# Kernel optimization log

Hardware: AMD Instinct MI355X
Metric: run time of the kernel (lower is better)

## Reference

```python
import jax, jax.numpy as jnp
import numpy as np

B, C, H, W = 8, 64, 256, 256


def setup_inputs() -> dict:
    key = jax.random.key(0)
    ks = jax.random.split(key, 7)
    return {
        "x": jax.random.normal(ks[0], (B, C, H, W), dtype=jnp.float32),
        "query_w": jax.random.normal(ks[1], (C, W, W), dtype=jnp.float32),
        "key_w": jax.random.normal(ks[2], (C, W, W), dtype=jnp.float32),
        "var_w": jax.random.normal(ks[3], (C, W, W), dtype=jnp.float32),
        "query_b": jax.random.normal(ks[4], (C, H, W), dtype=jnp.float32),
        "key_b": jax.random.normal(ks[5], (C, H, W), dtype=jnp.float32),
        "var_b": jax.random.normal(ks[6], (C, H, W), dtype=jnp.float32),
    }


def reference(x, query_w, key_w, var_w, query_b, key_b, var_b):
    # mode == 'horizontal': per-channel right-matmul over the W axis.
    # x: [B,C,H,W], *_w: [C,W,W] (broadcast over batch), *_b: [C,H,W].
    q = jnp.einsum("bchw,cwv->bchv", x, query_w) + query_b
    k = jnp.einsum("bchw,cwv->bchv", x, key_w) + key_b
    v = jnp.einsum("bchw,cwv->bchv", x, var_w) + var_b
    return jax.nn.softmax(q * k, axis=-1) * v
```

## Files before the change

kernel.cpp:

```cpp
#include <hip/hip_runtime.h>
#include <math.h>


#define Bn 8
#define Cn 64
#define Hn 256
#define Wn 256

typedef _Float16 f16x8 __attribute__((ext_vector_type(8)));
typedef _Float16 f16x4 __attribute__((ext_vector_type(4)));
typedef float    f32x16 __attribute__((ext_vector_type(16)));

#define MFMA(a, b, c) __builtin_amdgcn_mfma_f32_32x32x16_f16((a), (b), (c), 0, 0, 0)

#define WS_PLANE_H 4096
#define WS_NEED ((size_t)Cn * 16 * 5 * 8192)

#define FPL  8192
#define FBUF 40960

__device__ __forceinline__ void ldst16(const void* g, void* l) {
    __builtin_amdgcn_global_load_lds(
        (const __attribute__((address_space(1))) unsigned int*)g,
        (__attribute__((address_space(3))) unsigned int*)l, 16, 0, 0);
}

__device__ __forceinline__ void cvt_hilo(const float4 a, const float4 b,
                                         f16x8& hi, f16x8& lo) {
    float v[8] = {a.x, a.y, a.z, a.w, b.x, b.y, b.z, b.w};
#pragma unroll
    for (int e = 0; e < 8; ++e) {
        _Float16 hv = (_Float16)v[e];
        hi[e] = hv;
        lo[e] = (_Float16)(v[e] - (float)hv);
    }
}

__global__ __launch_bounds__(256) void prep_w(
    const float* __restrict__ wq, const float* __restrict__ wk,
    const float* __restrict__ wv, _Float16* __restrict__ wf)
{
    const int blk = blockIdx.x;
    const int kt  = blk & 15;
    const int c   = blk >> 4;
    const int n   = threadIdx.x;
    const int ntile = n >> 5;
    const int nl    = n & 31;

    _Float16* base = wf + (size_t)blk * 5 * WS_PLANE_H;
    const size_t woff = ((size_t)c * Wn + kt * 16) * Wn + n;

#pragma unroll
    for (int mat = 0; mat < 2; ++mat) {
        const float* Wp = (mat ? wk : wq) + woff;
        float w16[16];
#pragma unroll
        for (int r = 0; r < 16; ++r)
            w16[r] = Wp[(size_t)r * Wn];
        _Float16* hip = base + (mat * 2) * WS_PLANE_H + ntile * 512;
        _Float16* lop = hip + WS_PLANE_H;
#pragma unroll
        for (int h2 = 0; h2 < 2; ++h2) {
            f16x8 hi8, lo8;
#pragma unroll
            for (int e = 0; e < 8; ++e) {
                const float wv_ = w16[h2 * 8 + e];
                _Float16 hv = (_Float16)wv_;
                hi8[e] = hv;
                lo8[e] = (_Float16)(wv_ - (float)hv);
            }
            *(f16x8*)(hip + (h2 * 32 + nl) * 8) = hi8;
            *(f16x8*)(lop + (h2 * 32 + nl) * 8) = lo8;
        }
    }
    {
        const float* Wp = wv + woff;
        float w16[16];
#pragma unroll
        for (int r = 0; r < 16; ++r)
            w16[r] = Wp[(size_t)r * Wn];
        _Float16* vp = base + 4 * WS_PLANE_H + ntile * 512;
#pragma unroll
        for (int h2 = 0; h2 < 2; ++h2) {
            f16x8 hi8;
#pragma unroll
            for (int e = 0; e < 8; ++e)
                hi8[e] = (_Float16)w16[h2 * 8 + e];
            *(f16x8*)(vp + (h2 * 32 + nl) * 8) = hi8;
        }
    }
}

__global__ __launch_bounds__(512, 4) void axile_attn_fused(
    const float* __restrict__ x,
    const _Float16* __restrict__ wf,
    const float* __restrict__ bq,
    const float* __restrict__ bk,
    const float* __restrict__ bv,
    float* __restrict__ out)
{
    __shared__ __align__(16) char lds[2 * FBUF];

    const int tid  = threadIdx.x;
    const int ncol = tid >> 6;
    const int lane = tid & 63;
    const int h    = lane >> 5;
    const int l31  = lane & 31;

    const int blk = blockIdx.x;
    const int c   = blk & 63;
    const int j   = blk >> 6;
    const int b   = j & 7;
    const int h0  = (j >> 3) * 32;

    const float* xrow = x + ((size_t)(b * Cn + c) * Hn + h0 + l31) * Wn + h * 8;
    const _Float16* wfc = wf + (size_t)c * 16 * 5 * WS_PLANE_H;

    f32x16 accq, acck, accv;
#pragma unroll
    for (int r = 0; r < 16; ++r) {
        accq[r] = 0.f;
        acck[r] = 0.f;
        accv[r] = 0.f;
    }

#pragma unroll
    for (int p = 0; p < 5; ++p)
        ldst16(wfc + p * WS_PLANE_H + tid * 8, lds + p * FPL + tid * 16);
    f16x8 ah, al;
    {
        const float4 xa = *(const float4*)(xrow);
        const float4 xb = *(const float4*)(xrow + 4);
        cvt_hilo(xa, xb, ah, al);
    }
    __syncthreads();

    int curo = 0;
    for (int kt = 0; kt < 16; ++kt) {
        const int nxto = curo ^ FBUF;
        float4 xa, xb;
        if (kt < 15) {
            xa = *(const float4*)(xrow + (kt + 1) * 16);
            xb = *(const float4*)(xrow + (kt + 1) * 16 + 4);
            const _Float16* wsp = wfc + (size_t)(kt + 1) * 5 * WS_PLANE_H;
#pragma unroll
            for (int p = 0; p < 5; ++p)
                ldst16(wsp + p * WS_PLANE_H + tid * 8,
                       lds + nxto + p * FPL + tid * 16);
        }

        const char* bb = lds + curo + ncol * 1024 + lane * 16;
        const f16x8 bqh = *(const f16x8*)(bb + 0 * FPL);
        const f16x8 bql = *(const f16x8*)(bb + 1 * FPL);
        const f16x8 bkh = *(const f16x8*)(bb + 2 * FPL);
        const f16x8 bkl = *(const f16x8*)(bb + 3 * FPL);
        const f16x8 bvh = *(const f16x8*)(bb + 4 * FPL);

        accq = MFMA(ah, bqh, accq);
        accq = MFMA(al, bqh, accq);
        accq = MFMA(ah, bql, accq);
        acck = MFMA(ah, bkh, acck);
        acck = MFMA(al, bkh, acck);
        acck = MFMA(ah, bkl, acck);
        accv = MFMA(ah, bvh, accv);

        if (kt < 15)
            cvt_hilo(xa, xb, ah, al);
        __syncthreads();
        curo = nxto;
    }

    float* part    = (float*)lds;
    float* combmax = (float*)(lds + 1024);
    float* combsum = (float*)(lds + 1152);

#pragma unroll
    for (int r = 0; r < 16; ++r) {
        const int row = (r & 3) + 8 * (r >> 2) + 4 * h;
        const int hh  = h0 + row;
        const int vv  = ncol * 32 + l31;
        const size_t bidx = ((size_t)c * Hn + hh) * Wn + vv;
        const float qv = accq[r] + bq[bidx];
        const float kv = acck[r] + bk[bidx];
        accq[r] = qv * kv;
    }

#pragma unroll
    for (int r = 0; r < 16; ++r) {
        float m2 = accq[r];
#pragma unroll
        for (int off = 16; off > 0; off >>= 1)
            m2 = fmaxf(m2, __shfl_xor(m2, off, 64));
        if ((lane & 31) == r) {
            const int row = (r & 3) + 8 * (r >> 2) + 4 * h;
            part[ncol * 32 + row] = m2;
        }
    }
    __syncthreads();
    if (tid < 32) {
        float m = part[tid];
#pragma unroll
        for (int w = 1; w < 8; ++w)
            m = fmaxf(m, part[w * 32 + tid]);
        combmax[tid] = m;
    }
    __syncthreads();

#pragma unroll
    for (int r = 0; r < 16; ++r) {
        const int row = (r & 3) + 8 * (r >> 2) + 4 * h;
        const float mx = combmax[row];
        const float e0 = __expf(accq[r] - mx);
        accq[r] = e0;
        float ps = e0;
#pragma unroll
        for (int off = 16; off > 0; off >>= 1)
            ps += __shfl_xor(ps, off, 64);
        if ((lane & 31) == r)
            part[ncol * 32 + row] = ps;
    }
    __syncthreads();
    if (tid < 32) {
        float s = part[tid];
#pragma unroll
        for (int w = 1; w < 8; ++w)
            s += part[w * 32 + tid];
        combsum[tid] = s;
    }
    __syncthreads();

    float* obase = out + ((size_t)(b * Cn + c) * Hn) * Wn;
#pragma unroll
    for (int r = 0; r < 16; ++r) {
        const int row = (r & 3) + 8 * (r >> 2) + 4 * h;
        const float inv = 1.0f / combsum[row];
        const int hh = h0 + row;
        const int vv = ncol * 32 + l31;
        const size_t bidx = ((size_t)c * Hn + hh) * Wn + vv;
        const float vx = accv[r] + bv[bidx];
        obase[(size_t)hh * Wn + vv] = accq[r] * vx * inv;
    }
}

#define LDS_ALO 2048
#define LDS_B   4096

__global__ __launch_bounds__(512, 4) void axile_attn_mfma4(
    const float* __restrict__ x,
    const float* __restrict__ wq,
    const float* __restrict__ wk,
    const float* __restrict__ wv,
    const float* __restrict__ bq,
    const float* __restrict__ bk,
    const float* __restrict__ bv,
    float* __restrict__ out)
{
    __shared__ __align__(16) char lds[39424];

    const int tid  = threadIdx.x;
    const int ncol = tid >> 6;
    const int lane = tid & 63;
    const int h    = lane >> 5;
    const int l31  = lane & 31;

    const int blk = blockIdx.x;
    const int c   = blk & 63;
    const int j   = blk >> 6;
    const int b   = j & 7;
    const int h0  = (j >> 3) * 64;

    const float* xbase = x + ((size_t)(b * Cn + c) * Hn + h0) * Wn;
    const float* w_q = wq + (size_t)c * Wn * Wn;
    const float* w_k = wk + (size_t)c * Wn * Wn;
    const float* w_v = wv + (size_t)c * Wn * Wn;

    const int wkh = tid >> 8;
    const int n   = tid & 255;
    const int ntW = n >> 5;
    const int nl  = n & 31;
    const int wfo = ((wkh << 5) | nl) * 16;
    const int am    = tid >> 2;
    const int akq   = tid & 3;
    const int amt   = am >> 5;
    const int alc   = ((akq >> 1) << 5) | (am & 31);
    const int aboff = (akq & 1) * 8;

    f32x16 accq[2], acck[2];
#pragma unroll
    for (int mt = 0; mt < 2; ++mt)
#pragma unroll
        for (int r = 0; r < 16; ++r) {
            accq[mt][r] = 0.f;
            acck[mt][r] = 0.f;
        }

    for (int kt = 0; kt < 16; ++kt) {
        const int k0 = kt * 16;
        __syncthreads();
#pragma unroll
        for (int mat = 0; mat < 2; ++mat) {
            const float* Wp = mat ? w_k : w_q;
            const float* wrow = Wp + (size_t)(k0 + wkh * 8) * Wn + n;
            float w8[8];
#pragma unroll
            for (int r = 0; r < 8; ++r)
                w8[r] = wrow[(size_t)r * Wn];
            f16x8 hi8, lo8;
#pragma unroll
            for (int e = 0; e < 8; ++e) {
                const float wv_ = w8[e];
                _Float16 hv = (_Float16)wv_;
                hi8[e] = hv;
                lo8[e] = (_Float16)(wv_ - (float)hv);
            }
            char* dplane = lds + LDS_B + (mat * 2) * 8192 + ntW * 1024;
            *(f16x8*)(dplane + wfo) = hi8;
            *(f16x8*)(dplane + 8192 + wfo) = lo8;
        }
        if (tid < 256) {
            const float4 xx = *(const float4*)(xbase + (size_t)am * Wn + k0 + akq * 4);
            f16x4 hi4, lo4;
            _Float16 t0 = (_Float16)xx.x; hi4[0] = t0; lo4[0] = (_Float16)(xx.x - (float)t0);
            _Float16 t1 = (_Float16)xx.y; hi4[1] = t1; lo4[1] = (_Float16)(xx.y - (float)t1);
            _Float16 t2 = (_Float16)xx.z; hi4[2] = t2; lo4[2] = (_Float16)(xx.z - (float)t2);
            _Float16 t3 = (_Float16)xx.w; hi4[3] = t3; lo4[3] = (_Float16)(xx.w - (float)t3);
            *(f16x4*)(lds + amt * 1024 + alc * 16 + aboff) = hi4;
            *(f16x4*)(lds + LDS_ALO + amt * 1024 + alc * 16 + aboff) = lo4;
        }
        __syncthreads();

        f16x8 ah[2], al[2];
#pragma unroll
        for (int mt = 0; mt < 2; ++mt) {
            ah[mt] = *(const f16x8*)(lds + mt * 1024 + lane * 16);
            al[mt] = *(const f16x8*)(lds + LDS_ALO + mt * 1024 + lane * 16);
        }
        const char* bb = lds + LDS_B + ncol * 1024 + lane * 16;
        f16x8 bqh = *(const f16x8*)(bb + 0 * 8192);
        f16x8 bql = *(const f16x8*)(bb + 1 * 8192);
        f16x8 bkh = *(const f16x8*)(bb + 2 * 8192);
        f16x8 bkl = *(const f16x8*)(bb + 3 * 8192);
#pragma unroll
        for (int mt = 0; mt < 2; ++mt) {
            accq[mt] = MFMA(ah[mt], bqh, accq[mt]);
            accq[mt] = MFMA(al[mt], bqh, accq[mt]);
            accq[mt] = MFMA(ah[mt], bql, accq[mt]);
            acck[mt] = MFMA(ah[mt], bkh, acck[mt]);
            acck[mt] = MFMA(al[mt], bkh, acck[mt]);
            acck[mt] = MFMA(ah[mt], bkl, acck[mt]);
        }
    }

    float* part    = (float*)(lds + 36864);
    float* combmax = (float*)(lds + 36864 + 2048);
    float* combsum = (float*)(lds + 36864 + 2304);

#pragma unroll
    for (int mt = 0; mt < 2; ++mt)
#pragma unroll
        for (int r = 0; r < 16; ++r) {
            const int rl = (r & 3) + 8 * (r >> 2) + 4 * h;
            const int hh = h0 + mt * 32 + rl;
            const int vv = ncol * 32 + l31;
            const size_t bidx = ((size_t)c * Hn + hh) * Wn + vv;
            const float qv = accq[mt][r] + bq[bidx];
            const float kv = acck[mt][r] + bk[bidx];
            accq[mt][r] = qv * kv;
        }

#pragma unroll
    for (int mt = 0; mt < 2; ++mt)
#pragma unroll
        for (int r = 0; r < 16; ++r) {
            float m2 = accq[mt][r];
#pragma unroll
            for (int off = 16; off > 0; off >>= 1)
                m2 = fmaxf(m2, __shfl_xor(m2, off, 64));
            if ((lane & 15) == r && ((lane >> 4) & 1) == mt) {
                const int rl  = (r & 3) + 8 * (r >> 2) + 4 * h;
                const int row = mt * 32 + rl;
                part[ncol * 64 + row] = m2;
            }
        }
    __syncthreads();
    if (tid < 64) {
        float m = part[tid];
#pragma unroll
        for (int w = 1; w < 8; ++w)
            m = fmaxf(m, part[w * 64 + tid]);
        combmax[tid] = m;
    }
    __syncthreads();

#pragma unroll
    for (int mt = 0; mt < 2; ++mt)
#pragma unroll
        for (int r = 0; r < 16; ++r) {
            const int rl  = (r & 3) + 8 * (r >> 2) + 4 * h;
            const int row = mt * 32 + rl;
            const float mx = combmax[row];
            const float e0 = __expf(accq[mt][r] - mx);
            accq[mt][r] = e0;
            float ps = e0;
#pragma unroll
            for (int off = 16; off > 0; off >>= 1)
                ps += __shfl_xor(ps, off, 64);
            if ((lane & 15) == r && ((lane >> 4) & 1) == mt)
                part[ncol * 64 + row] = ps;
        }
    __syncthreads();
    if (tid < 64) {
        float s = part[tid];
#pragma unroll
        for (int w = 1; w < 8; ++w)
            s += part[w * 64 + tid];
        combsum[tid] = s;
    }

    f32x16 accv[2];
#pragma unroll
    for (int mt = 0; mt < 2; ++mt)
#pragma unroll
        for (int r = 0; r < 16; ++r)
            accv[mt][r] = 0.f;

    for (int kt = 0; kt < 16; ++kt) {
        const int k0 = kt * 16;
        __syncthreads();
        {
            const float* wrow = w_v + (size_t)(k0 + wkh * 8) * Wn + n;
            float w8[8];
#pragma unroll
            for (int r = 0; r < 8; ++r)
                w8[r] = wrow[(size_t)r * Wn];
            f16x8 hi8;
#pragma unroll
            for (int e = 0; e < 8; ++e)
                hi8[e] = (_Float16)w8[e];
            *(f16x8*)(lds + LDS_B + ntW * 1024 + wfo) = hi8;
        }
        if (tid < 256) {
            const float4 xx = *(const float4*)(xbase + (size_t)am * Wn + k0 + akq * 4);
            f16x4 hi4;
            hi4[0] = (_Float16)xx.x;
            hi4[1] = (_Float16)xx.y;
            hi4[2] = (_Float16)xx.z;
            hi4[3] = (_Float16)xx.w;
            *(f16x4*)(lds + amt * 1024 + alc * 16 + aboff) = hi4;
        }
        __syncthreads();

        f16x8 ah[2];
#pragma unroll
        for (int mt = 0; mt < 2; ++mt)
            ah[mt] = *(const f16x8*)(lds + mt * 1024 + lane * 16);
        f16x8 bvh = *(const f16x8*)(lds + LDS_B + ncol * 1024 + lane * 16);
#pragma unroll
        for (int mt = 0; mt < 2; ++mt)
            accv[mt] = MFMA(ah[mt], bvh, accv[mt]);
    }

    float* obase = out + ((size_t)(b * Cn + c) * Hn) * Wn;
#pragma unroll
    for (int mt = 0; mt < 2; ++mt)
#pragma unroll
        for (int r = 0; r < 16; ++r) {
            const int rl  = (r & 3) + 8 * (r >> 2) + 4 * h;
            const int row = mt * 32 + rl;
            const float inv = 1.0f / combsum[row];
            const int hh = h0 + row;
            const int vv = ncol * 32 + l31;
            const size_t bidx = ((size_t)c * Hn + hh) * Wn + vv;
            const float vx = accv[mt][r] + bv[bidx];
            obase[(size_t)hh * Wn + vv] = accq[mt][r] * vx * inv;
        }
}

extern "C" void kernel_launch(void* const* d_in, const int* in_sizes, int n_in,
                              void* d_out, int out_size, void* d_ws, size_t ws_size,
                              hipStream_t stream) {
    (void)in_sizes; (void)n_in; (void)out_size;
    const float* x  = (const float*)d_in[0];
    const float* wq = (const float*)d_in[1];
    const float* wk = (const float*)d_in[2];
    const float* wv = (const float*)d_in[3];
    const float* bq = (const float*)d_in[4];
    const float* bk = (const float*)d_in[5];
    const float* bv = (const float*)d_in[6];
    float* out = (float*)d_out;

    if (d_ws != nullptr && ws_size >= WS_NEED) {
        hipLaunchKernelGGL(prep_w, dim3(Cn * 16), dim3(256), 0, stream,
                           wq, wk, wv, (_Float16*)d_ws);
        hipLaunchKernelGGL(axile_attn_fused, dim3(Bn * 8 * Cn), dim3(512), 0, stream,
                           x, (const _Float16*)d_ws, bq, bk, bv, out);
    } else {
        hipLaunchKernelGGL(axile_attn_mfma4, dim3(Bn * 4 * Cn), dim3(512), 0, stream,
                           x, wq, wk, wv, bq, bk, bv, out);
    }
}
```

Before: 549.0 us.

## Use 1024-thread blocks with 64-row tiles and triple-buffered weight prefetch

The fused kernel now uses 1024 threads covering 64 rows per block, so each staged weight tile is shared by two row groups and global weight traffic per output halves. The double buffer becomes a three-stage ring filled two tiles ahead, with explicit vmcnt waits and raw s_barrier in place of full __syncthreads. The aim is to hide global-to-LDS latency and cut redundant weight loads. The cost is 120KB of LDS per block, which limits residency to one block per CU, plus fragile hand-written waitcnt logic.

```diff
diff --git a/kernel.cpp b/kernel.cpp
--- a/kernel.cpp
+++ b/kernel.cpp
@@ -16,8 +16,7 @@
 #define WS_PLANE_H 4096
 #define WS_NEED ((size_t)Cn * 16 * 5 * 8192)
 
-#define FPL  8192
-#define FBUF 40960
+#define FTILE 40960
 
 __device__ __forceinline__ void ldst16(const void* g, void* l) {
     __builtin_amdgcn_global_load_lds(
@@ -91,7 +90,7 @@
     }
 }
 
-__global__ __launch_bounds__(512, 4) void axile_attn_fused(
+__global__ __launch_bounds__(1024, 4) void axile_attn_pipe(
     const float* __restrict__ x,
     const _Float16* __restrict__ wf,
     const float* __restrict__ bq,
@@ -99,22 +98,29 @@
     const float* __restrict__ bv,
     float* __restrict__ out)
 {
-    __shared__ __align__(16) char lds[2 * FBUF];
-
-    const int tid  = threadIdx.x;
-    const int ncol = tid >> 6;
-    const int lane = tid & 63;
-    const int h    = lane >> 5;
-    const int l31  = lane & 31;
+    __shared__ __align__(16) char lds[3 * FTILE];
+
+    const int tid   = threadIdx.x;
+    const int lane  = tid & 63;
+    const int h     = lane >> 5;
+    const int l31   = lane & 31;
+    const int wv_id = tid >> 6;
+    const int ncol  = wv_id & 7;
+    const int mt    = wv_id >> 3;
 
     const int blk = blockIdx.x;
     const int c   = blk & 63;
     const int j   = blk >> 6;
     const int b   = j & 7;
-    const int h0  = (j >> 3) * 32;
-
-    const float* xrow = x + ((size_t)(b * Cn + c) * Hn + h0 + l31) * Wn + h * 8;
-    const _Float16* wfc = wf + (size_t)c * 16 * 5 * WS_PLANE_H;
+    const int h0  = (j >> 3) * 64;
+
+    const float* xrow = x + ((size_t)(b * Cn + c) * Hn + h0 + mt * 32 + l31) * Wn + h * 8;
+    const char*  wfc  = (const char*)(wf + (size_t)c * 16 * 5 * WS_PLANE_H);
+
+    const bool halfw = (tid < 512);
+    const int  so0 = tid * 16;
+    const int  so1 = 16384 + tid * 16;
+    const int  so2 = 32768 + tid * 16;
 
     f32x16 accq, acck, accv;
 #pragma unroll
@@ -124,37 +130,44 @@
         accv[r] = 0.f;
     }
 
-#pragma unroll
-    for (int p = 0; p < 5; ++p)
-        ldst16(wfc + p * WS_PLANE_H + tid * 8, lds + p * FPL + tid * 16);
     f16x8 ah, al;
     {
         const float4 xa = *(const float4*)(xrow);
         const float4 xb = *(const float4*)(xrow + 4);
+        ldst16(wfc + so0, lds + so0);
+        ldst16(wfc + so1, lds + so1);
+        if (halfw) ldst16(wfc + so2, lds + so2);
+        const char* s1 = wfc + FTILE;
+        ldst16(s1 + so0, lds + FTILE + so0);
+        ldst16(s1 + so1, lds + FTILE + so1);
+        if (halfw) ldst16(s1 + so2, lds + FTILE + so2);
         cvt_hilo(xa, xb, ah, al);
     }
-    __syncthreads();
-
-    int curo = 0;
+    if (halfw) asm volatile("s_waitcnt vmcnt(3)" ::: "memory");
+    else       asm volatile("s_waitcnt vmcnt(2)" ::: "memory");
+    __builtin_amdgcn_s_barrier();
+    __builtin_amdgcn_sched_barrier(0);
+
+    int o_cur = 0, o_nxt = FTILE, o_sta = 2 * FTILE;
     for (int kt = 0; kt < 16; ++kt) {
-        const int nxto = curo ^ FBUF;
-        float4 xa, xb;
+        float4 ya, yb;
         if (kt < 15) {
-            xa = *(const float4*)(xrow + (kt + 1) * 16);
-            xb = *(const float4*)(xrow + (kt + 1) * 16 + 4);
-            const _Float16* wsp = wfc + (size_t)(kt + 1) * 5 * WS_PLANE_H;
-#pragma unroll
-            for (int p = 0; p < 5; ++p)
-                ldst16(wsp + p * WS_PLANE_H + tid * 8,
-                       lds + nxto + p * FPL + tid * 16);
-        }
-
-        const char* bb = lds + curo + ncol * 1024 + lane * 16;
-        const f16x8 bqh = *(const f16x8*)(bb + 0 * FPL);
-        const f16x8 bql = *(const f16x8*)(bb + 1 * FPL);
-        const f16x8 bkh = *(const f16x8*)(bb + 2 * FPL);
-        const f16x8 bkl = *(const f16x8*)(bb + 3 * FPL);
-        const f16x8 bvh = *(const f16x8*)(bb + 4 * FPL);
+            ya = *(const float4*)(xrow + (kt + 1) * 16);
+            yb = *(const float4*)(xrow + (kt + 1) * 16 + 4);
+        }
+        if (kt < 14) {
+            const char* ssrc = wfc + (size_t)(kt + 2) * FTILE;
+            ldst16(ssrc + so0, lds + o_sta + so0);
+            ldst16(ssrc + so1, lds + o_sta + so1);
+            if (halfw) ldst16(ssrc + so2, lds + o_sta + so2);
+        }
+
+        const char* bb = lds + o_cur + ncol * 1024 + lane * 16;
+        const f16x8 bqh = *(const f16x8*)(bb);
+        const f16x8 bql = *(const f16x8*)(bb + 8192);
+        const f16x8 bkh = *(const f16x8*)(bb + 16384);
+        const f16x8 bkl = *(const f16x8*)(bb + 24576);
+        const f16x8 bvh = *(const f16x8*)(bb + 32768);
 
         accq = MFMA(ah, bqh, accq);
         accq = MFMA(al, bqh, accq);
@@ -165,21 +178,28 @@
         accv = MFMA(ah, bvh, accv);
 
         if (kt < 15)
-            cvt_hilo(xa, xb, ah, al);
-        __syncthreads();
-        curo = nxto;
+            cvt_hilo(ya, yb, ah, al);
+
+        if (kt < 14) {
+            if (halfw) asm volatile("s_waitcnt vmcnt(3)" ::: "memory");
+            else       asm volatile("s_waitcnt vmcnt(2)" ::: "memory");
+        } else if (kt == 14) {
+            asm volatile("s_waitcnt vmcnt(0)" ::: "memory");
+        }
+        __builtin_amdgcn_s_barrier();
+        __builtin_amdgcn_sched_barrier(0);
+        const int t = o_cur; o_cur = o_nxt; o_nxt = o_sta; o_sta = t;
     }
 
     float* part    = (float*)lds;
-    float* combmax = (float*)(lds + 1024);
-    float* combsum = (float*)(lds + 1152);
+    float* combmax = (float*)(lds + 2048);
+    float* combsum = (float*)(lds + 2304);
 
 #pragma unroll
     for (int r = 0; r < 16; ++r) {
-        const int row = (r & 3) + 8 * (r >> 2) + 4 * h;
-        const int hh  = h0 + row;
+        const int row = mt * 32 + (r & 3) + 8 * (r >> 2) + 4 * h;
         const int vv  = ncol * 32 + l31;
-        const size_t bidx = ((size_t)c * Hn + hh) * Wn + vv;
+        const size_t bidx = ((size_t)c * Hn + h0 + row) * Wn + vv;
         const float qv = accq[r] + bq[bidx];
         const float kv = acck[r] + bk[bidx];
         accq[r] = qv * kv;
@@ -192,23 +212,23 @@
         for (int off = 16; off > 0; off >>= 1)
             m2 = fmaxf(m2, __shfl_xor(m2, off, 64));
         if ((lane & 31) == r) {
-            const int row = (r & 3) + 8 * (r >> 2) + 4 * h;
-            part[ncol * 32 + row] = m2;
-        }
-    }
-    __syncthreads();
-    if (tid < 32) {
+            const int row = mt * 32 + (r & 3) + 8 * (r >> 2) + 4 * h;
+            part[ncol * 64 + row] = m2;
+        }
+    }
+    __syncthreads();
+    if (tid < 64) {
         float m = part[tid];
 #pragma unroll
         for (int w = 1; w < 8; ++w)
-            m = fmaxf(m, part[w * 32 + tid]);
+            m = fmaxf(m, part[w * 64 + tid]);
         combmax[tid] = m;
     }
     __syncthreads();
 
 #pragma unroll
     for (int r = 0; r < 16; ++r) {
-        const int row = (r & 3) + 8 * (r >> 2) + 4 * h;
+        const int row = mt * 32 + (r & 3) + 8 * (r >> 2) + 4 * h;
         const float mx = combmax[row];
         const float e0 = __expf(accq[r] - mx);
         accq[r] = e0;
@@ -217,14 +237,14 @@
         for (int off = 16; off > 0; off >>= 1)
             ps += __shfl_xor(ps, off, 64);
         if ((lane & 31) == r)
-            part[ncol * 32 + row] = ps;
-    }
-    __syncthreads();
-    if (tid < 32) {
+            part[ncol * 64 + row] = ps;
+    }
+    __syncthreads();
+    if (tid < 64) {
         float s = part[tid];
 #pragma unroll
         for (int w = 1; w < 8; ++w)
-            s += part[w * 32 + tid];
+            s += part[w * 64 + tid];
         combsum[tid] = s;
     }
     __syncthreads();
@@ -232,7 +252,7 @@
     float* obase = out + ((size_t)(b * Cn + c) * Hn) * Wn;
 #pragma unroll
     for (int r = 0; r < 16; ++r) {
-        const int row = (r & 3) + 8 * (r >> 2) + 4 * h;
+        const int row = mt * 32 + (r & 3) + 8 * (r >> 2) + 4 * h;
         const float inv = 1.0f / combsum[row];
         const int hh = h0 + row;
         const int vv = ncol * 32 + l31;
@@ -287,11 +307,11 @@
 
     f32x16 accq[2], acck[2];
 #pragma unroll
-    for (int mt = 0; mt < 2; ++mt)
+    for (int mtx = 0; mtx < 2; ++mtx)
 #pragma unroll
         for (int r = 0; r < 16; ++r) {
-            accq[mt][r] = 0.f;
-            acck[mt][r] = 0.f;
+            accq[mtx][r] = 0.f;
+            acck[mtx][r] = 0.f;
         }
 
     for (int kt = 0; kt < 16; ++kt) {
@@ -331,9 +351,9 @@
 
         f16x8 ah[2], al[2];
 #pragma unroll
-        for (int mt = 0; mt < 2; ++mt) {
-            ah[mt] = *(const f16x8*)(lds + mt * 1024 + lane * 16);
-            al[mt] = *(const f16x8*)(lds + LDS_ALO + mt * 1024 + lane * 16);
+        for (int mtx = 0; mtx < 2; ++mtx) {
+            ah[mtx] = *(const f16x8*)(lds + mtx * 1024 + lane * 16);
+            al[mtx] = *(const f16x8*)(lds + LDS_ALO + mtx * 1024 + lane * 16);
         }
         const char* bb = lds + LDS_B + ncol * 1024 + lane * 16;
         f16x8 bqh = *(const f16x8*)(bb + 0 * 8192);
@@ -341,13 +361,13 @@
         f16x8 bkh = *(const f16x8*)(bb + 2 * 8192);
         f16x8 bkl = *(const f16x8*)(bb + 3 * 8192);
 #pragma unroll
-        for (int mt = 0; mt < 2; ++mt) {
-            accq[mt] = MFMA(ah[mt], bqh, accq[mt]);
-            accq[mt] = MFMA(al[mt], bqh, accq[mt]);
-            accq[mt] = MFMA(ah[mt], bql, accq[mt]);
-            acck[mt] = MFMA(ah[mt], bkh, acck[mt]);
-            acck[mt] = MFMA(al[mt], bkh, acck[mt]);
-            acck[mt] = MFMA(ah[mt], bkl, acck[mt]);
+        for (int mtx = 0; mtx < 2; ++mtx) {
+            accq[mtx] = MFMA(ah[mtx], bqh, accq[mtx]);
+            accq[mtx] = MFMA(al[mtx], bqh, accq[mtx]);
+            accq[mtx] = MFMA(ah[mtx], bql, accq[mtx]);
+            acck[mtx] = MFMA(ah[mtx], bkh, acck[mtx]);
+            acck[mtx] = MFMA(al[mtx], bkh, acck[mtx]);
+            acck[mtx] = MFMA(ah[mtx], bkl, acck[mtx]);
         }
     }
 
@@ -356,29 +376,29 @@
     float* combsum = (float*)(lds + 36864 + 2304);
 
 #pragma unroll
-    for (int mt = 0; mt < 2; ++mt)
+    for (int mtx = 0; mtx < 2; ++mtx)
 #pragma unroll
         for (int r = 0; r < 16; ++r) {
             const int rl = (r & 3) + 8 * (r >> 2) + 4 * h;
-            const int hh = h0 + mt * 32 + rl;
+            const int hh = h0 + mtx * 32 + rl;
             const int vv = ncol * 32 + l31;
             const size_t bidx = ((size_t)c * Hn + hh) * Wn + vv;
-            const float qv = accq[mt][r] + bq[bidx];
-            const float kv = acck[mt][r] + bk[bidx];
-            accq[mt][r] = qv * kv;
-        }
-
-#pragma unroll
-    for (int mt = 0; mt < 2; ++mt)
+            const float qv = accq[mtx][r] + bq[bidx];
+            const float kv = acck[mtx][r] + bk[bidx];
+            accq[mtx][r] = qv * kv;
+        }
+
+#pragma unroll
+    for (int mtx = 0; mtx < 2; ++mtx)
 #pragma unroll
         for (int r = 0; r < 16; ++r) {
-            float m2 = accq[mt][r];
+            float m2 = accq[mtx][r];
 #pragma unroll
             for (int off = 16; off > 0; off >>= 1)
                 m2 = fmaxf(m2, __shfl_xor(m2, off, 64));
-            if ((lane & 15) == r && ((lane >> 4) & 1) == mt) {
+            if ((lane & 15) == r && ((lane >> 4) & 1) == mtx) {
                 const int rl  = (r & 3) + 8 * (r >> 2) + 4 * h;
-                const int row = mt * 32 + rl;
+                const int row = mtx * 32 + rl;
                 part[ncol * 64 + row] = m2;
             }
         }
@@ -393,19 +413,19 @@
     __syncthreads();
 
 #pragma unroll
-    for (int mt = 0; mt < 2; ++mt)
+    for (int mtx = 0; mtx < 2; ++mtx)
 #pragma unroll
         for (int r = 0; r < 16; ++r) {
             const int rl  = (r & 3) + 8 * (r >> 2) + 4 * h;
-            const int row = mt * 32 + rl;
+            const int row = mtx * 32 + rl;
             const float mx = combmax[row];
-            const float e0 = __expf(accq[mt][r] - mx);
-            accq[mt][r] = e0;
+            const float e0 = __expf(accq[mtx][r] - mx);
+            accq[mtx][r] = e0;
             float ps = e0;
 #pragma unroll
             for (int off = 16; off > 0; off >>= 1)
                 ps += __shfl_xor(ps, off, 64);
-            if ((lane & 15) == r && ((lane >> 4) & 1) == mt)
+            if ((lane & 15) == r && ((lane >> 4) & 1) == mtx)
                 part[ncol * 64 + row] = ps;
         }
     __syncthreads();
@@ -419,10 +439,10 @@
 
     f32x16 accv[2];
 #pragma unroll
-    for (int mt = 0; mt < 2; ++mt)
+    for (int mtx = 0; mtx < 2; ++mtx)
 #pragma unroll
         for (int r = 0; r < 16; ++r)
-            accv[mt][r] = 0.f;
+            accv[mtx][r] = 0.f;
 
     for (int kt = 0; kt < 16; ++kt) {
         const int k0 = kt * 16;
@@ -452,27 +472,27 @@
 
         f16x8 ah[2];
 #pragma unroll
-        for (int mt = 0; mt < 2; ++mt)
-            ah[mt] = *(const f16x8*)(lds + mt * 1024 + lane * 16);
+        for (int mtx = 0; mtx < 2; ++mtx)
+            ah[mtx] = *(const f16x8*)(lds + mtx * 1024 + lane * 16);
         f16x8 bvh = *(const f16x8*)(lds + LDS_B + ncol * 1024 + lane * 16);
 #pragma unroll
-        for (int mt = 0; mt < 2; ++mt)
-            accv[mt] = MFMA(ah[mt], bvh, accv[mt]);
+        for (int mtx = 0; mtx < 2; ++mtx)
+            accv[mtx] = MFMA(ah[mtx], bvh, accv[mtx]);
     }
 
     float* obase = out + ((size_t)(b * Cn + c) * Hn) * Wn;
 #pragma unroll
-    for (int mt = 0; mt < 2; ++mt)
+    for (int mtx = 0; mtx < 2; ++mtx)
 #pragma unroll
         for (int r = 0; r < 16; ++r) {
             const int rl  = (r & 3) + 8 * (r >> 2) + 4 * h;
-            const int row = mt * 32 + rl;
+            const int row = mtx * 32 + rl;
             const float inv = 1.0f / combsum[row];
             const int hh = h0 + row;
             const int vv = ncol * 32 + l31;
             const size_t bidx = ((size_t)c * Hn + hh) * Wn + vv;
-            const float vx = accv[mt][r] + bv[bidx];
-            obase[(size_t)hh * Wn + vv] = accq[mt][r] * vx * inv;
+            const float vx = accv[mtx][r] + bv[bidx];
+            obase[(size_t)hh * Wn + vv] = accq[mtx][r] * vx * inv;
         }
 }
 
@@ -492,7 +512,7 @@
     if (d_ws != nullptr && ws_size >= WS_NEED) {
         hipLaunchKernelGGL(prep_w, dim3(Cn * 16), dim3(256), 0, stream,
                            wq, wk, wv, (_Float16*)d_ws);
-        hipLaunchKernelGGL(axile_attn_fused, dim3(Bn * 8 * Cn), dim3(512), 0, stream,
+        hipLaunchKernelGGL(axile_attn_pipe, dim3(Bn * 4 * Cn), dim3(1024), 0, stream,
                            x, (const _Float16*)d_ws, bq, bk, bv, out);
     } else {
         hipLaunchKernelGGL(axile_attn_mfma4, dim3(Bn * 4 * Cn), dim3(512), 0, stream,
```

New measurement: 559.3 us. No clear change (+1.9%).
